# Performance work log

Hardware: AMD Instinct MI355X
Metric: run time of the kernel (lower is better)

Reference implementation:

```python
import jax, jax.numpy as jnp
import numpy as np

T, B, DICO, EMB, LAT = 256, 64, 8192, 256, 256


def setup_inputs() -> dict:
    key = jax.random.key(0)
    ks = jax.random.split(key, 7)
    s_emb = 1.0 / np.sqrt(DICO)
    s_enc = 1.0 / np.sqrt(EMB + LAT)
    return {
        "x": jax.random.normal(ks[0], (T, B, DICO), dtype=jnp.float32),
        "h": jax.random.normal(ks[1], (B, LAT), dtype=jnp.float32),
        "W_emb": jax.random.uniform(ks[2], (DICO, EMB), jnp.float32, -s_emb, s_emb),
        "b_emb": jax.random.uniform(ks[3], (EMB,), jnp.float32, -s_emb, s_emb),
        "W_enc": jax.random.uniform(ks[4], (EMB + LAT, LAT), jnp.float32, -s_enc, s_enc),
        "b_enc": jax.random.uniform(ks[5], (LAT,), jnp.float32, -s_enc, s_enc),
    }


def reference(x, h, W_emb, b_emb, W_enc, b_enc):
    # embedding: [T,B,DICO] @ [DICO,EMB] -> [T,B,EMB]
    xe = jnp.einsum('tbd,de->tbe', x, W_emb) + b_emb
    # split encoder weight into x-part and h-part: cat(x,h)@W == x@Wx + h@Wh
    Wx, Wh = W_enc[:EMB], W_enc[EMB:]
    # hoist the per-step x projection out of the scan (no h dependence)
    xp = jnp.einsum('tbe,el->tbl', xe, Wx) + b_enc  # [T,B,LAT]

    def step(h, xp_t):
        h_new = jnp.tanh(xp_t + h @ Wh)
        return h_new, h_new

    _, hs = jax.lax.scan(step, h, xp)
    return hs  # [T,B,LAT]
```

## Files before the change

### kernel.cpp

```cpp
#include <hip/hip_runtime.h>
#include <hip/hip_bf16.h>
#include <stdint.h>

#define T_DIM 256
#define B_DIM 64
#define DICO  8192
#define EMB   256
#define LAT   256
#define M_DIM (T_DIM*B_DIM)

#define BM 64
#define BN 256
#define BK 64
#define KSPLIT 2
#define KCHUNK (DICO/KSPLIT)
#define NKS (KCHUNK/BK)

typedef short  bf16x8 __attribute__((ext_vector_type(8)));
typedef float  f32x4  __attribute__((ext_vector_type(4)));
typedef _Float16 f16x2 __attribute__((ext_vector_type(2)));

__device__ __forceinline__ ushort f2bf(float f) {
  uint32_t u = __float_as_uint(f);
  u += 0x7FFFu + ((u >> 16) & 1u);
  return (ushort)(u >> 16);
}

__device__ __forceinline__ void glds16(const void* g, void* l) {
  __builtin_amdgcn_global_load_lds(
      (const __attribute__((address_space(1))) uint32_t*)g,
      (__attribute__((address_space(3))) uint32_t*)l, 16, 0, 0);
}

__global__ void wct_kernel(const float* __restrict__ Wemb, const float* __restrict__ Wenc,
                           ushort* __restrict__ wct) {
  const int n  = threadIdx.x;
  const int d0 = blockIdx.x * 32;
  __shared__ float we[32 * 256];
  __shared__ float tr[32 * 257];
  #pragma unroll
  for (int r = 0; r < 32; ++r) we[r*256 + n] = Wemb[(size_t)(d0 + r)*EMB + n];
  __syncthreads();
  float acc[32];
  #pragma unroll
  for (int d = 0; d < 32; ++d) acc[d] = 0.f;
  #pragma unroll 4
  for (int e = 0; e < 256; ++e) {
    float wv = Wenc[e*LAT + n];
    #pragma unroll
    for (int d = 0; d < 32; ++d) acc[d] += we[d*256 + e] * wv;
  }
  #pragma unroll
  for (int d = 0; d < 32; ++d) tr[d*257 + n] = acc[d];
  __syncthreads();
  const int nn0 = n >> 2, kc = n & 3;
  #pragma unroll
  for (int p = 0; p < 4; ++p) {
    int nn = p*64 + nn0;
    bf16x8 v;
    #pragma unroll
    for (int j = 0; j < 8; ++j) v[j] = (short)f2bf(tr[(kc*8 + j)*257 + nn]);
    *(bf16x8*)(wct + (size_t)nn*DICO + d0 + kc*8) = v;
  }
}

__global__ void __launch_bounds__(256, 2) gemm_kernel(const float* __restrict__ x,
                                                      const ushort* __restrict__ wct,
                                                      float* __restrict__ xp) {
  __shared__ __align__(16) ushort sA[BM * BK];
  __shared__ __align__(16) ushort sB[BN * BK];
  const int tid = threadIdx.x;
  const int bid = blockIdx.x;
  const int swzb = (bid & 7) * 64 + (bid >> 3);
  const int mt = swzb & 255, ksp = swzb >> 8;
  const size_t rowbase = (size_t)mt * BM;
  const int kbase = ksp * KCHUNK;

  const int lane = tid & 63, wid = tid >> 6;
  const int l15 = lane & 15, lc = lane >> 4;

  const int r0 = tid >> 2, c0 = tid & 3;
  const float* ag = x + (rowbase + r0) * (size_t)DICO + kbase + c0 * 16;
  const int sx0 = (((2*c0    ) ^ (r0 & 7)) * 16);
  const int sx1 = (((2*c0 + 1) ^ (r0 & 7)) * 16);

  const int sw0 = (((    lc) ^ (l15 & 7)) * 16);
  const int sw1 = (((4 + lc) ^ (l15 & 7)) * 16);

  const char* wb = (const char*)wct;
  const size_t kb2 = (size_t)kbase * 2;

  const int brow_s = (tid >> 3);
  const int bslot_s = tid & 7;

  f32x4 acc[4][4];
  #pragma unroll
  for (int m = 0; m < 4; ++m)
    #pragma unroll
    for (int n = 0; n < 4; ++n) acc[m][n] = (f32x4){0.f, 0.f, 0.f, 0.f};

  float4 av[4];

  auto loadA = [&](int kofs) {
    #pragma unroll
    for (int q = 0; q < 4; ++q) av[q] = *(const float4*)(ag + kofs + q * 4);
  };
  auto stageB = [&](int kofs) {
    #pragma unroll
    for (int r = 0; r < 8; ++r) {
      const int row = r * 32 + brow_s;
      const int srcslot = bslot_s ^ (row & 7);
      glds16(wb + (size_t)row * (DICO * 2) + kb2 + (size_t)kofs * 2 + srcslot * 16,
             (char*)sB + r * 4096 + tid * 16);
    }
  };
  auto storeA = [&]() {
    const float4 a0 = av[0], a1 = av[1], a2 = av[2], a3 = av[3];
    bf16x8 w0, w1;
    w0[0]=(short)f2bf(a0.x); w0[1]=(short)f2bf(a0.y); w0[2]=(short)f2bf(a0.z); w0[3]=(short)f2bf(a0.w);
    w0[4]=(short)f2bf(a1.x); w0[5]=(short)f2bf(a1.y); w0[6]=(short)f2bf(a1.z); w0[7]=(short)f2bf(a1.w);
    w1[0]=(short)f2bf(a2.x); w1[1]=(short)f2bf(a2.y); w1[2]=(short)f2bf(a2.z); w1[3]=(short)f2bf(a2.w);
    w1[4]=(short)f2bf(a3.x); w1[5]=(short)f2bf(a3.y); w1[6]=(short)f2bf(a3.z); w1[7]=(short)f2bf(a3.w);
    char* base = (char*)sA + r0 * 128;
    *(bf16x8*)(base + sx0) = w0;
    *(bf16x8*)(base + sx1) = w1;
  };
  auto compute = [&]() {
    bf16x8 bfr[4][2];
    #pragma unroll
    for (int n = 0; n < 4; ++n) {
      const char* bb = (const char*)sB + (wid*64 + n*16 + l15) * 128;
      bfr[n][0] = *(const bf16x8*)(bb + sw0);
      bfr[n][1] = *(const bf16x8*)(bb + sw1);
    }
    #pragma unroll
    for (int m = 0; m < 4; ++m) {
      const char* ab = (const char*)sA + (m*16 + l15) * 128;
      bf16x8 a0 = *(const bf16x8*)(ab + sw0);
      bf16x8 a1 = *(const bf16x8*)(ab + sw1);
      #pragma unroll
      for (int n = 0; n < 4; ++n) {
        acc[m][n] = __builtin_amdgcn_mfma_f32_16x16x32_bf16(a0, bfr[n][0], acc[m][n], 0, 0, 0);
        acc[m][n] = __builtin_amdgcn_mfma_f32_16x16x32_bf16(a1, bfr[n][1], acc[m][n], 0, 0, 0);
      }
    }
  };

  loadA(0);
  for (int ks = 0; ks < NKS; ++ks) {
    __syncthreads();
    storeA();
    stageB(ks * BK);
    __syncthreads();
    if (ks + 1 < NKS) loadA((ks + 1) * BK);
    compute();
  }

  float* xpo = xp + ((size_t)ksp * M_DIM + rowbase) * LAT;
  #pragma unroll
  for (int m = 0; m < 4; ++m)
    #pragma unroll
    for (int n = 0; n < 4; ++n)
      #pragma unroll
      for (int j = 0; j < 4; ++j)
        xpo[(size_t)(m*16 + lc*4 + j) * LAT + wid*64 + n*16 + l15] = acc[m][n][j];
}

__global__ void __launch_bounds__(256, 1) rnn_kernel(const float* __restrict__ xp,
                           const float* __restrict__ h0, const float* __restrict__ Wenc,
                           const float* __restrict__ bemb, const float* __restrict__ benc,
                           float* __restrict__ out) {
  const int b = blockIdx.x, l = threadIdx.x;
  __shared__ __align__(16) uint32_t hbuf[2][128];
  float bc = benc[l];
  #pragma unroll 8
  for (int e = 0; e < 256; ++e) bc += bemb[e] * Wenc[e*LAT + l];
  f16x2 wh[128];
  #pragma unroll
  for (int j = 0; j < 128; ++j) {
    f16x2 w;
    w[0] = (_Float16)Wenc[(size_t)(EMB + 2*j    )*LAT + l];
    w[1] = (_Float16)Wenc[(size_t)(EMB + 2*j + 1)*LAT + l];
    wh[j] = w;
  }
  ((_Float16*)&hbuf[0][0])[l] = (_Float16)h0[(size_t)b*LAT + l];
  __syncthreads();
  const float* xpb = xp + (size_t)b*LAT + l;
  float*       ob  = out + (size_t)b*LAT + l;
  const size_t ST = (size_t)B_DIM * LAT;
  const size_t PO = (size_t)M_DIM * LAT;
  float xa0 = xpb[0],  xa1 = xpb[PO];
  float xb0 = xpb[ST], xb1 = xpb[ST + PO];
  float xc0 = 0.f, xc1 = 0.f;
  for (int t = 0; t < T_DIM; ++t) {
    if (t + 2 < T_DIM) {
      size_t ni = (size_t)(t + 2) * ST;
      xc0 = xpb[ni]; xc1 = xpb[ni + PO];
    }
    const uint32_t* hc = &hbuf[t & 1][0];
    float s0=0.f,s1=0.f,s2=0.f,s3=0.f,s4=0.f,s5=0.f,s6=0.f,s7=0.f;
    #pragma unroll
    for (int q = 0; q < 16; ++q) {
      uint4 hv0 = *(const uint4*)(hc + q*8);
      uint4 hv1 = *(const uint4*)(hc + q*8 + 4);
      s0 = __builtin_amdgcn_fdot2(wh[q*8+0], __builtin_bit_cast(f16x2, hv0.x), s0, false);
      s1 = __builtin_amdgcn_fdot2(wh[q*8+1], __builtin_bit_cast(f16x2, hv0.y), s1, false);
      s2 = __builtin_amdgcn_fdot2(wh[q*8+2], __builtin_bit_cast(f16x2, hv0.z), s2, false);
      s3 = __builtin_amdgcn_fdot2(wh[q*8+3], __builtin_bit_cast(f16x2, hv0.w), s3, false);
      s4 = __builtin_amdgcn_fdot2(wh[q*8+4], __builtin_bit_cast(f16x2, hv1.x), s4, false);
      s5 = __builtin_amdgcn_fdot2(wh[q*8+5], __builtin_bit_cast(f16x2, hv1.y), s5, false);
      s6 = __builtin_amdgcn_fdot2(wh[q*8+6], __builtin_bit_cast(f16x2, hv1.z), s6, false);
      s7 = __builtin_amdgcn_fdot2(wh[q*8+7], __builtin_bit_cast(f16x2, hv1.w), s7, false);
    }
    float pre = (xa0 + xa1) + bc + (((s0+s1)+(s2+s3)) + ((s4+s5)+(s6+s7)));
    float ax = fabsf(pre);
    float e2 = __expf(-2.f * ax);
    float r  = __fdividef(1.f - e2, 1.f + e2);
    float hn = (pre < 0.f) ? -r : r;
    ob[(size_t)t * ST] = hn;
    ((_Float16*)&hbuf[(t + 1) & 1][0])[l] = (_Float16)hn;
    __builtin_amdgcn_sched_barrier(0);
    asm volatile("s_waitcnt lgkmcnt(0)" ::: "memory");
    __builtin_amdgcn_s_barrier();
    __builtin_amdgcn_sched_barrier(0);
    xa0 = xb0; xa1 = xb1; xb0 = xc0; xb1 = xc1;
  }
}

extern "C" void kernel_launch(void* const* d_in, const int* in_sizes, int n_in,
                              void* d_out, int out_size, void* d_ws, size_t ws_size,
                              hipStream_t stream) {
  const float* x    = (const float*)d_in[0];
  const float* h0   = (const float*)d_in[1];
  const float* Wemb = (const float*)d_in[2];
  const float* bemb = (const float*)d_in[3];
  const float* Wenc = (const float*)d_in[4];
  const float* benc = (const float*)d_in[5];
  float* out = (float*)d_out;

  ushort* wct = (ushort*)d_ws;
  float*  xp  = (float*)((char*)d_ws + ((size_t)4 << 20));

  wct_kernel<<<256, 256, 0, stream>>>(Wemb, Wenc, wct);
  gemm_kernel<<<512, 256, 0, stream>>>(x, wct, xp);
  rnn_kernel<<<64, 256, 0, stream>>>(xp, h0, Wenc, bemb, benc, out);
}
```

Baseline: 660.4 us.

## Double-buffer LDS tiles and prefetch two stages ahead in GEMM kernel

Doubles the shared-memory A and B tiles so the next B tile (via global-to-LDS loads) and the A tile two steps ahead are fetched while MFMA compute runs on the current buffer. Each iteration needs one barrier instead of two, with explicit vmcnt/lgkmcnt waits. The intent is to hide global load latency behind compute. In exchange, LDS use per block doubles, which may limit occupancy, and the hand-placed waitcnt values have to match the exact number of outstanding loads.

```diff
diff --git a/kernel.cpp b/kernel.cpp
--- a/kernel.cpp
+++ b/kernel.cpp
@@ -67,8 +67,8 @@
 __global__ void __launch_bounds__(256, 2) gemm_kernel(const float* __restrict__ x,
                                                       const ushort* __restrict__ wct,
                                                       float* __restrict__ xp) {
-  __shared__ __align__(16) ushort sA[BM * BK];
-  __shared__ __align__(16) ushort sB[BN * BK];
+  __shared__ __align__(16) ushort sA[2][BM * BK];
+  __shared__ __align__(16) ushort sB[2][BN * BK];
   const int tid = threadIdx.x;
   const int bid = blockIdx.x;
   const int swzb = (bid & 7) * 64 + (bid >> 3);
@@ -99,43 +99,39 @@
     #pragma unroll
     for (int n = 0; n < 4; ++n) acc[m][n] = (f32x4){0.f, 0.f, 0.f, 0.f};
 
-  float4 av[4];
-
-  auto loadA = [&](int kofs) {
-    #pragma unroll
-    for (int q = 0; q < 4; ++q) av[q] = *(const float4*)(ag + kofs + q * 4);
-  };
-  auto stageB = [&](int kofs) {
+  float4 avP[4], avQ[4];
+
+  auto stageB = [&](int buf, int kofs) {
     #pragma unroll
     for (int r = 0; r < 8; ++r) {
       const int row = r * 32 + brow_s;
       const int srcslot = bslot_s ^ (row & 7);
       glds16(wb + (size_t)row * (DICO * 2) + kb2 + (size_t)kofs * 2 + srcslot * 16,
-             (char*)sB + r * 4096 + tid * 16);
-    }
-  };
-  auto storeA = [&]() {
+             (char*)&sB[buf][0] + r * 4096 + tid * 16);
+    }
+  };
+  auto storeA = [&](int buf, const float4* av) {
     const float4 a0 = av[0], a1 = av[1], a2 = av[2], a3 = av[3];
     bf16x8 w0, w1;
     w0[0]=(short)f2bf(a0.x); w0[1]=(short)f2bf(a0.y); w0[2]=(short)f2bf(a0.z); w0[3]=(short)f2bf(a0.w);
     w0[4]=(short)f2bf(a1.x); w0[5]=(short)f2bf(a1.y); w0[6]=(short)f2bf(a1.z); w0[7]=(short)f2bf(a1.w);
     w1[0]=(short)f2bf(a2.x); w1[1]=(short)f2bf(a2.y); w1[2]=(short)f2bf(a2.z); w1[3]=(short)f2bf(a2.w);
     w1[4]=(short)f2bf(a3.x); w1[5]=(short)f2bf(a3.y); w1[6]=(short)f2bf(a3.z); w1[7]=(short)f2bf(a3.w);
-    char* base = (char*)sA + r0 * 128;
+    char* base = (char*)&sA[buf][0] + r0 * 128;
     *(bf16x8*)(base + sx0) = w0;
     *(bf16x8*)(base + sx1) = w1;
   };
-  auto compute = [&]() {
+  auto compute = [&](int buf) {
     bf16x8 bfr[4][2];
     #pragma unroll
     for (int n = 0; n < 4; ++n) {
-      const char* bb = (const char*)sB + (wid*64 + n*16 + l15) * 128;
+      const char* bb = (const char*)&sB[buf][0] + (wid*64 + n*16 + l15) * 128;
       bfr[n][0] = *(const bf16x8*)(bb + sw0);
       bfr[n][1] = *(const bf16x8*)(bb + sw1);
     }
     #pragma unroll
     for (int m = 0; m < 4; ++m) {
-      const char* ab = (const char*)sA + (m*16 + l15) * 128;
+      const char* ab = (const char*)&sA[buf][0] + (m*16 + l15) * 128;
       bf16x8 a0 = *(const bf16x8*)(ab + sw0);
       bf16x8 a1 = *(const bf16x8*)(ab + sw1);
       #pragma unroll
@@ -146,14 +142,33 @@
     }
   };
 
-  loadA(0);
-  for (int ks = 0; ks < NKS; ++ks) {
-    __syncthreads();
-    storeA();
-    stageB(ks * BK);
-    __syncthreads();
-    if (ks + 1 < NKS) loadA((ks + 1) * BK);
-    compute();
+  auto body = [&](int k, float4* avC, float4* avL) {
+    const int p = k & 1;
+    const int kB = (k + 1 < NKS ? k + 1 : NKS - 1) * BK;
+    const int kA = (k + 2 < NKS ? k + 2 : NKS - 1) * BK;
+    stageB(p ^ 1, kB);
+    asm volatile("" ::: "memory");
+    #pragma unroll
+    for (int q = 0; q < 4; ++q) avL[q] = *(const float4*)(ag + kA + q * 4);
+    storeA(p ^ 1, avC);
+    compute(p);
+    asm volatile("s_waitcnt vmcnt(4)" ::: "memory");
+    asm volatile("s_waitcnt lgkmcnt(0)" ::: "memory");
+    __builtin_amdgcn_s_barrier();
+    __builtin_amdgcn_sched_barrier(0);
+  };
+
+  stageB(0, 0);
+  #pragma unroll
+  for (int q = 0; q < 4; ++q) avP[q] = *(const float4*)(ag + 0   + q * 4);
+  #pragma unroll
+  for (int q = 0; q < 4; ++q) avQ[q] = *(const float4*)(ag + BK  + q * 4);
+  storeA(0, avP);
+  __syncthreads();
+
+  for (int k = 0; k < NKS; k += 2) {
+    body(k,     avQ, avP);
+    body(k + 1, avP, avQ);
   }
 
   float* xpo = xp + ((size_t)ksp * M_DIM + rowbase) * LAT;
```

New measurement: 658.9 us. Within noise of the previous version (-0.2%).
